# Performance work log

Measured on AMD Instinct MI355X. Metric: run time of the kernel, lower is better.

## Reference

```python
import jax, jax.numpy as jnp
import numpy as np

# 5x5 neighborhood offsets as (dx, dy), row-major as in the original delta list
DELTA = [(dx, dy) for dy in (-2, -1, 0, 1, 2) for dx in (-2, -1, 0, 1, 2)]
BN_EPS = 1e-5


def _conv(x, w, padding):
    return jax.lax.conv_general_dilated(
        x, w, window_strides=(1, 1), padding=padding,
        dimension_numbers=('NCHW', 'OIHW', 'NCHW'))


def setup_inputs() -> dict:
    key = jax.random.key(0)
    ks = jax.random.split(key, 4)
    B, C, H, W = 128, 256, 24, 24
    source_feature = jax.random.normal(ks[0], (B, C, H, W), jnp.float32)
    detection_feature = jax.random.normal(ks[1], (B, C, H, W), jnp.float32)
    w1 = jax.random.normal(ks[2], (256, 512, 3, 3), jnp.float32) * 0.02
    b1 = jnp.zeros((256,), jnp.float32)
    bn_gamma = jnp.ones((256,), jnp.float32)
    bn_beta = jnp.zeros((256,), jnp.float32)
    bn_mean = jnp.zeros((256,), jnp.float32)
    bn_var = jnp.ones((256,), jnp.float32)
    w2 = jax.random.normal(ks[3], (25, 256, 1, 1), jnp.float32) * 0.05
    b2 = jnp.zeros((25,), jnp.float32)
    return dict(source_feature=source_feature, detection_feature=detection_feature,
                w1=w1, b1=b1, bn_gamma=bn_gamma, bn_beta=bn_beta,
                bn_mean=bn_mean, bn_var=bn_var, w2=w2, b2=b2)


def reference(source_feature, detection_feature, w1, b1, bn_gamma, bn_beta,
              bn_mean, bn_var, w2, b2):
    B, C, H, W = source_feature.shape
    # kernel_pre: Conv3x3(512->256, pad 1) + BN + ReLU + Conv1x1(256->25)
    concat_f = jnp.concatenate([source_feature, detection_feature], axis=1)  # [B,512,H,W]
    x = _conv(concat_f, w1, ((1, 1), (1, 1))) + b1[None, :, None, None]
    inv = bn_gamma / jnp.sqrt(bn_var + BN_EPS)
    x = x * inv[None, :, None, None] + (bn_beta - bn_mean * inv)[None, :, None, None]
    x = jax.nn.relu(x)
    logits = _conv(x, w2, ((0, 0), (0, 0))) + b2[None, :, None, None]  # [B,25,H,W]
    # per-pixel softmax over the 25 neighborhood taps
    kmaps = jax.nn.softmax(logits, axis=1)  # [B,25,H,W]
    # propagate: softmax-weighted 5x5 neighbor gather-sum; out-of-bounds taps
    # contribute zero (matches the skipped-boundary terms in the original loop)
    padded = jnp.pad(source_feature, ((0, 0), (0, 0), (2, 2), (2, 2)))
    prop = jnp.zeros_like(source_feature)
    for order, (dx, dy) in enumerate(DELTA):
        shifted = padded[:, :, 2 + dy:2 + dy + H, 2 + dx:2 + dx + W]  # [B,C,H,W]
        prop = prop + shifted * kmaps[:, order][:, None]  # broadcast over C
    return prop
```

## Files before the change

kernel.cpp:

```cpp
#include <hip/hip_runtime.h>
#include <hip/hip_bf16.h>
#include <stdint.h>

#define BATCH 128
#define CIN   256
#define CCAT  512
#define HH    24
#define WW    24
#define HP    26
#define WP    26
#define COUT  256
#define KDIM  4608
#define NPIX  576
#define MDIM  73728
#define NORD  25

typedef __attribute__((ext_vector_type(8))) short bf16x8;
typedef __attribute__((ext_vector_type(4))) float f32x4;

__device__ __forceinline__ unsigned short f2bf(float v) {
    union { float f; unsigned u; } x; x.f = v;
    unsigned r = x.u + 0x7fffu + ((x.u >> 16) & 1u);
    return (unsigned short)(r >> 16);
}
__device__ __forceinline__ float bf_lo(unsigned w) {
    union { unsigned u; float f; } x; x.u = w << 16; return x.f;
}
__device__ __forceinline__ float bf_hi(unsigned w) {
    union { unsigned u; float f; } x; x.u = w & 0xffff0000u; return x.f;
}

__device__ __forceinline__ void async_copy16(const void* gsrc, void* ldst) {
    __builtin_amdgcn_global_load_lds(
        (const __attribute__((address_space(1))) unsigned int*)gsrc,
        (__attribute__((address_space(3))) unsigned int*)ldst, 16, 0, 0);
}

#define PTILE 192
#define LSTR  72
__global__ __launch_bounds__(256) void prep_transpose(
        const float* __restrict__ src, const float* __restrict__ det,
        unsigned short* __restrict__ apad) {
    __shared__ unsigned short lds[PTILE * LSTR];
    int pt = blockIdx.x;
    int cg = blockIdx.y;
    int b  = blockIdx.z;
    int c0 = cg * 64;
    int p0 = pt * PTILE;
    const float* inp = (c0 < CIN)
        ? (src + ((long)b * CIN + c0) * NPIX)
        : (det + ((long)b * CIN + (c0 - CIN)) * NPIX);
    int tid = threadIdx.x;

    #pragma unroll
    for (int it = 0; it < 12; it++) {
        int l  = it * 256 + tid;
        int cq = l / PTILE;
        int px = l - cq * PTILE;
        const float* pb = inp + (long)cq * 4 * NPIX + p0 + px;
        unsigned short v0 = f2bf(pb[0 * NPIX]);
        unsigned short v1 = f2bf(pb[1 * NPIX]);
        unsigned short v2 = f2bf(pb[2 * NPIX]);
        unsigned short v3 = f2bf(pb[3 * NPIX]);
        uint2 w;
        w.x = (unsigned)v0 | ((unsigned)v1 << 16);
        w.y = (unsigned)v2 | ((unsigned)v3 << 16);
        *(uint2*)&lds[px * LSTR + cq * 4] = w;
    }
    __syncthreads();

    #pragma unroll
    for (int it = 0; it < 6; it++) {
        int l   = it * 256 + tid;
        int px  = l >> 3;
        int ch8 = l & 7;
        uint4 w = *(const uint4*)&lds[px * LSTR + ch8 * 8];
        int p  = p0 + px;
        int y  = p / WW, x = p - y * WW;
        long o = (((long)b * HP + (y + 1)) * WP + (x + 1)) * CCAT + c0 + ch8 * 8;
        *(uint4*)(apad + o) = w;
    }
}

__global__ __launch_bounds__(256) void zero_halo(unsigned short* __restrict__ apad) {
    int t = blockIdx.x * 256 + threadIdx.x;
    int ch8 = t & 63;
    int r   = t >> 6;
    int hp  = r % 100;
    int b   = r / 100;
    int y, x;
    if (hp < 26)      { y = 0;       x = hp; }
    else if (hp < 52) { y = 25;      x = hp - 26; }
    else if (hp < 76) { y = hp - 51; x = 0; }
    else              { y = hp - 75; x = 25; }
    long o = (((long)b * HP + y) * WP + x) * CCAT + ch8 * 8;
    *(uint4*)(apad + o) = (uint4){0u, 0u, 0u, 0u};
}

__global__ __launch_bounds__(256) void prep_w(
        const float* __restrict__ w1, const float* __restrict__ b1,
        const float* __restrict__ gam, const float* __restrict__ bet,
        const float* __restrict__ mu, const float* __restrict__ var,
        unsigned short* __restrict__ bt,
        float* __restrict__ scale, float* __restrict__ shift) {
    int idx = blockIdx.x * 256 + threadIdx.x;
    if (idx < COUT * KDIM) {
        int n = idx / KDIM;
        int k = idx - n * KDIM;
        int s = k >> 9;
        int ci = k & 511;
        int ky = s / 3, kx = s - ky * 3;
        float v = w1[(((long)n * 512 + ci) * 3 + ky) * 3 + kx];
        bt[idx] = f2bf(v);
    }
    if (blockIdx.x == 0 && threadIdx.x < COUT) {
        int c = threadIdx.x;
        float inv = gam[c] * rsqrtf(var[c] + 1e-5f);
        scale[c] = inv;
        shift[c] = (b1[c] - mu[c]) * inv + bet[c];
    }
}

#define ABUF_SH 12288
#define BUF_SH  20480
#define STAGE_A(j, nb, soff) \
    async_copy16(apad + aSrc[j] + (soff), (void*)&lds[(nb)*BUF_SH + (j)*4096 + w*512])
#define STAGE_B(j, nb, koff) \
    async_copy16(bt + bSrc[j] + (koff), (void*)&lds[(nb)*BUF_SH + ABUF_SH + (j)*4096 + w*512])
#define BAR()  __builtin_amdgcn_s_barrier()
#define WAITV2() { asm volatile("s_waitcnt vmcnt(2)" ::: "memory"); }
#define WAITV0() { asm volatile("s_waitcnt vmcnt(0)" ::: "memory"); }
#define WAITL()  { asm volatile("s_waitcnt lgkmcnt(0)" ::: "memory"); __builtin_amdgcn_sched_barrier(0); }

__global__ __launch_bounds__(512, 2) void conv1_gemm(
        const unsigned short* __restrict__ apad,
        const unsigned short* __restrict__ bt,
        const float* __restrict__ scale, const float* __restrict__ shift,
        unsigned short* __restrict__ xout) {
    __shared__ unsigned short lds[40960];
    const int tid  = threadIdx.x;
    const int w    = tid >> 6;
    const int lane = tid & 63;
    const int wr = w >> 2, wc = w & 3;
    const int fr = lane & 15, ls = lane >> 4;

    const int Lb = blockIdx.x;
    const int logical = (Lb & 7) * 96 + (Lb >> 3);
    const int n0 = (logical & 1) * 128;
    const long m0 = (long)(logical >> 1) * 192;

    const int rowq = tid >> 3;
    const int sl   = (tid & 7) ^ (rowq & 7);
    long aSrc[3], bSrc[2];
    #pragma unroll
    for (int j = 0; j < 3; j++) {
        int r = j * 64 + rowq;
        long m = m0 + r;
        int b  = (int)(m / NPIX);
        int rr = (int)(m - (long)b * NPIX);
        int y = rr / WW, x = rr - y * WW;
        aSrc[j] = (((long)b * HP + y) * WP + x) * (long)CCAT + sl * 8;
    }
    #pragma unroll
    for (int j = 0; j < 2; j++)
        bSrc[j] = (long)(n0 + j * 64 + rowq) * KDIM + sl * 8;

    const int rb   = fr & 7;
    const int csw0 = ((ls    ) ^ rb) << 4;
    const int csw1 = ((ls + 4) ^ rb) << 4;
    const int aBase = (wr * 96 + fr) * 128;
    const int bBase = 24576 + (wc * 32 + fr) * 128;

    f32x4 acc[6][2];
    #pragma unroll
    for (int i = 0; i < 6; i++)
        #pragma unroll
        for (int j = 0; j < 2; j++) acc[i][j] = (f32x4){0.f, 0.f, 0.f, 0.f};

    STAGE_B(0, 0, 0); STAGE_B(1, 0, 0);
    STAGE_A(0, 0, 0); STAGE_A(1, 0, 0); STAGE_A(2, 0, 0);

    bf16x8 afr[3], bfr[2];
    int nb = 0;
    for (int kt = 0; kt < 71; kt++) {
        const int ktn = kt + 1;
        const int seg = ktn >> 3;
        const int ky = seg / 3, kx = seg - ky * 3;
        const long soff = (long)(ky * WP + kx) * CCAT + (ktn & 7) * 64;
        const long koff = (long)ktn * 64;
        const int pb = nb ^ 1;
        const char* L = (const char*)lds + nb * (BUF_SH * 2);

        STAGE_B(0, pb, koff); STAGE_B(1, pb, koff);
        WAITV2();
        BAR();
        #pragma unroll
        for (int n = 0; n < 2; n++)
            bfr[n] = *(const bf16x8*)(L + bBase + n * 2048 + csw0);
        #pragma unroll
        for (int m = 0; m < 3; m++)
            afr[m] = *(const bf16x8*)(L + aBase + m * 2048 + csw0);
        WAITL();
        __builtin_amdgcn_s_setprio(1);
        #pragma unroll
        for (int m = 0; m < 3; m++)
            #pragma unroll
            for (int n = 0; n < 2; n++)
                acc[m][n] = __builtin_amdgcn_mfma_f32_16x16x32_bf16(afr[m], bfr[n], acc[m][n], 0, 0, 0);
        __builtin_amdgcn_s_setprio(0);
        BAR();

        #pragma unroll
        for (int m = 0; m < 3; m++)
            afr[m] = *(const bf16x8*)(L + aBase + (3 + m) * 2048 + csw0);
        STAGE_A(0, pb, soff); STAGE_A(1, pb, soff); STAGE_A(2, pb, soff);
        WAITL();
        __builtin_amdgcn_s_setprio(1);
        #pragma unroll
        for (int m = 0; m < 3; m++)
            #pragma unroll
            for (int n = 0; n < 2; n++)
                acc[3 + m][n] = __builtin_amdgcn_mfma_f32_16x16x32_bf16(afr[m], bfr[n], acc[3 + m][n], 0, 0, 0);
        __builtin_amdgcn_s_setprio(0);
        BAR();

        #pragma unroll
        for (int n = 0; n < 2; n++)
            bfr[n] = *(const bf16x8*)(L + bBase + n * 2048 + csw1);
        #pragma unroll
        for (int m = 0; m < 3; m++)
            afr[m] = *(const bf16x8*)(L + aBase + m * 2048 + csw1);
        WAITL();
        __builtin_amdgcn_s_setprio(1);
        #pragma unroll
        for (int m = 0; m < 3; m++)
            #pragma unroll
            for (int n = 0; n < 2; n++)
                acc[m][n] = __builtin_amdgcn_mfma_f32_16x16x32_bf16(afr[m], bfr[n], acc[m][n], 0, 0, 0);
        __builtin_amdgcn_s_setprio(0);
        BAR();

        #pragma unroll
        for (int m = 0; m < 3; m++)
            afr[m] = *(const bf16x8*)(L + aBase + (3 + m) * 2048 + csw1);
        WAITL();
        __builtin_amdgcn_s_setprio(1);
        #pragma unroll
        for (int m = 0; m < 3; m++)
            #pragma unroll
            for (int n = 0; n < 2; n++)
                acc[3 + m][n] = __builtin_amdgcn_mfma_f32_16x16x32_bf16(afr[m], bfr[n], acc[3 + m][n], 0, 0, 0);
        __builtin_amdgcn_s_setprio(0);
        BAR();

        nb ^= 1;
    }

    {
        const char* L = (const char*)lds + nb * (BUF_SH * 2);
        WAITV0();
        BAR();
        #pragma unroll
        for (int n = 0; n < 2; n++)
            bfr[n] = *(const bf16x8*)(L + bBase + n * 2048 + csw0);
        #pragma unroll
        for (int m = 0; m < 3; m++)
            afr[m] = *(const bf16x8*)(L + aBase + m * 2048 + csw0);
        WAITL();
        #pragma unroll
        for (int m = 0; m < 3; m++)
            #pragma unroll
            for (int n = 0; n < 2; n++)
                acc[m][n] = __builtin_amdgcn_mfma_f32_16x16x32_bf16(afr[m], bfr[n], acc[m][n], 0, 0, 0);
        #pragma unroll
        for (int m = 0; m < 3; m++)
            afr[m] = *(const bf16x8*)(L + aBase + (3 + m) * 2048 + csw0);
        WAITL();
        #pragma unroll
        for (int m = 0; m < 3; m++)
            #pragma unroll
            for (int n = 0; n < 2; n++)
                acc[3 + m][n] = __builtin_amdgcn_mfma_f32_16x16x32_bf16(afr[m], bfr[n], acc[3 + m][n], 0, 0, 0);
        #pragma unroll
        for (int n = 0; n < 2; n++)
            bfr[n] = *(const bf16x8*)(L + bBase + n * 2048 + csw1);
        #pragma unroll
        for (int m = 0; m < 3; m++)
            afr[m] = *(const bf16x8*)(L + aBase + m * 2048 + csw1);
        WAITL();
        #pragma unroll
        for (int m = 0; m < 3; m++)
            #pragma unroll
            for (int n = 0; n < 2; n++)
                acc[m][n] = __builtin_amdgcn_mfma_f32_16x16x32_bf16(afr[m], bfr[n], acc[m][n], 0, 0, 0);
        #pragma unroll
        for (int m = 0; m < 3; m++)
            afr[m] = *(const bf16x8*)(L + aBase + (3 + m) * 2048 + csw1);
        WAITL();
        #pragma unroll
        for (int m = 0; m < 3; m++)
            #pragma unroll
            for (int n = 0; n < 2; n++)
                acc[3 + m][n] = __builtin_amdgcn_mfma_f32_16x16x32_bf16(afr[m], bfr[n], acc[3 + m][n], 0, 0, 0);
    }

    #pragma unroll
    for (int n = 0; n < 2; n++) {
        int col = n0 + wc * 32 + n * 16 + fr;
        float sc = scale[col], sh = shift[col];
        #pragma unroll
        for (int m = 0; m < 6; m++) {
            long rbase = m0 + wr * 96 + m * 16 + ls * 4;
            #pragma unroll
            for (int j = 0; j < 4; j++) {
                float v = acc[m][n][j] * sc + sh;
                v = v > 0.f ? v : 0.f;
                xout[(rbase + j) * COUT + col] = f2bf(v);
            }
        }
    }
}

__global__ __launch_bounds__(256) void conv2_softmax(
        const unsigned short* __restrict__ x, const float* __restrict__ w2,
        const float* __restrict__ b2, float* __restrict__ kmaps) {
    __shared__ float w2s[NORD * 256];
    __shared__ float b2s[NORD];
    for (int i = threadIdx.x; i < NORD * 256; i += 256) w2s[i] = w2[i];
    if (threadIdx.x < NORD) b2s[threadIdx.x] = b2[threadIdx.x];
    __syncthreads();
    long pix = (long)blockIdx.x * 256 + threadIdx.x;
    float acc[NORD];
    #pragma unroll
    for (int o = 0; o < NORD; o++) acc[o] = b2s[o];
    const unsigned short* xr = x + pix * COUT;
    for (int kc = 0; kc < 32; kc++) {
        uint4 raw = *(const uint4*)(xr + kc * 8);
        float xf[8];
        xf[0] = bf_lo(raw.x); xf[1] = bf_hi(raw.x);
        xf[2] = bf_lo(raw.y); xf[3] = bf_hi(raw.y);
        xf[4] = bf_lo(raw.z); xf[5] = bf_hi(raw.z);
        xf[6] = bf_lo(raw.w); xf[7] = bf_hi(raw.w);
        #pragma unroll
        for (int o = 0; o < NORD; o++) {
            const float* wrow = &w2s[o * 256 + kc * 8];
            float4 wa = *(const float4*)(wrow);
            float4 wb = *(const float4*)(wrow + 4);
            acc[o] += xf[0] * wa.x + xf[1] * wa.y + xf[2] * wa.z + xf[3] * wa.w
                    + xf[4] * wb.x + xf[5] * wb.y + xf[6] * wb.z + xf[7] * wb.w;
        }
    }
    float mx = acc[0];
    #pragma unroll
    for (int o = 1; o < NORD; o++) mx = fmaxf(mx, acc[o]);
    float s = 0.f;
    #pragma unroll
    for (int o = 0; o < NORD; o++) { acc[o] = expf(acc[o] - mx); s += acc[o]; }
    float inv = 1.f / s;
    float* kout = kmaps + pix * NORD;
    #pragma unroll
    for (int o = 0; o < NORD; o++) kout[o] = acc[o] * inv;
}

__global__ __launch_bounds__(576) void propagate(
        const float* __restrict__ src, const float* __restrict__ kmaps,
        float* __restrict__ out) {
    __shared__ float sm[28 * 28];
    int b  = blockIdx.y;
    int cg = blockIdx.x;
    int tid = threadIdx.x;
    int y = tid / 24, x = tid - y * 24;
    float km[NORD];
    const float* kp = kmaps + ((long)b * NPIX + tid) * NORD;
    #pragma unroll
    for (int o = 0; o < NORD; o++) km[o] = kp[o];
    for (int c = 0; c < 16; c++) {
        int cc = cg * 16 + c;
        const float* sp = src + ((long)b * CIN + cc) * NPIX;
        __syncthreads();
        for (int t = tid; t < 28 * 28; t += 576) {
            int yy = t / 28, xx = t - yy * 28;
            float v = 0.f;
            if (yy >= 2 && yy < 26 && xx >= 2 && xx < 26)
                v = sp[(yy - 2) * 24 + (xx - 2)];
            sm[t] = v;
        }
        __syncthreads();
        float a = 0.f;
        #pragma unroll
        for (int o = 0; o < NORD; o++) {
            int dy = o / 5 - 2, dx = o % 5 - 2;
            a += km[o] * sm[(y + 2 + dy) * 28 + (x + 2 + dx)];
        }
        out[((long)b * CIN + cc) * NPIX + tid] = a;
    }
}

extern "C" void kernel_launch(void* const* d_in, const int* in_sizes, int n_in,
                              void* d_out, int out_size, void* d_ws, size_t ws_size,
                              hipStream_t stream) {
    const float* src = (const float*)d_in[0];
    const float* det = (const float*)d_in[1];
    const float* w1  = (const float*)d_in[2];
    const float* b1  = (const float*)d_in[3];
    const float* gam = (const float*)d_in[4];
    const float* bet = (const float*)d_in[5];
    const float* mu  = (const float*)d_in[6];
    const float* var = (const float*)d_in[7];
    const float* w2  = (const float*)d_in[8];
    const float* b2  = (const float*)d_in[9];
    float* out = (float*)d_out;

    char* ws = (char*)d_ws;
    size_t off = 0;
    unsigned short* apad = (unsigned short*)(ws + off); off += (size_t)BATCH * HP * WP * CCAT * 2;
    unsigned short* bt   = (unsigned short*)(ws + off); off += (size_t)COUT * KDIM * 2;
    unsigned short* xbuf = (unsigned short*)(ws + off); off += (size_t)MDIM * COUT * 2;
    float* kmaps = (float*)(ws + off); off += (size_t)MDIM * NORD * 4;
    float* scale = (float*)(ws + off); off += 1024;
    float* shift = (float*)(ws + off); off += 1024;

    zero_halo<<<3200, 256, 0, stream>>>(apad);
    prep_transpose<<<dim3(3, 8, BATCH), 256, 0, stream>>>(src, det, apad);
    prep_w<<<4608, 256, 0, stream>>>(w1, b1, gam, bet, mu, var, bt, scale, shift);
    conv1_gemm<<<768, 512, 0, stream>>>(apad, bt, scale, shift, xbuf);
    conv2_softmax<<<288, 256, 0, stream>>>(xbuf, w2, b2, kmaps);
    propagate<<<dim3(16, BATCH), 576, 0, stream>>>(src, kmaps, out);
}
```

Measured before the change: 358.7 us.

## Fold halo zeroing into prep, transpose kmaps layout, batch propagate channels

Halo zeroing moves into the prep_transpose kernel, which removes one launch. kmaps is now stored order-major so that per-pixel reads in propagate coalesce. propagate stages 8 channels per shared-memory round with 64 channels per block, cutting barriers and raising memory-level parallelism. In exchange the grid shrinks to 512 blocks and shared memory use grows, which may reduce occupancy.

```diff
diff --git a/kernel.cpp b/kernel.cpp
--- a/kernel.cpp
+++ b/kernel.cpp
@@ -52,6 +52,24 @@
         : (det + ((long)b * CIN + (c0 - CIN)) * NPIX);
     int tid = threadIdx.x;
 
+    if (pt == 0) {
+        #pragma unroll
+        for (int it = 0; it < 4; it++) {
+            int t = it * 256 + tid;
+            if (t < 800) {
+                int ch8 = t & 7;
+                int hp  = t >> 3;
+                int y, x;
+                if (hp < 26)      { y = 0;       x = hp; }
+                else if (hp < 52) { y = 25;      x = hp - 26; }
+                else if (hp < 76) { y = hp - 51; x = 0; }
+                else              { y = hp - 75; x = 25; }
+                long o = (((long)b * HP + y) * WP + x) * CCAT + c0 + ch8 * 8;
+                *(uint4*)(apad + o) = (uint4){0u, 0u, 0u, 0u};
+            }
+        }
+    }
+
     #pragma unroll
     for (int it = 0; it < 12; it++) {
         int l  = it * 256 + tid;
@@ -80,21 +98,6 @@
         long o = (((long)b * HP + (y + 1)) * WP + (x + 1)) * CCAT + c0 + ch8 * 8;
         *(uint4*)(apad + o) = w;
     }
-}
-
-__global__ __launch_bounds__(256) void zero_halo(unsigned short* __restrict__ apad) {
-    int t = blockIdx.x * 256 + threadIdx.x;
-    int ch8 = t & 63;
-    int r   = t >> 6;
-    int hp  = r % 100;
-    int b   = r / 100;
-    int y, x;
-    if (hp < 26)      { y = 0;       x = hp; }
-    else if (hp < 52) { y = 25;      x = hp - 26; }
-    else if (hp < 76) { y = hp - 51; x = 0; }
-    else              { y = hp - 75; x = 25; }
-    long o = (((long)b * HP + y) * WP + x) * CCAT + ch8 * 8;
-    *(uint4*)(apad + o) = (uint4){0u, 0u, 0u, 0u};
 }
 
 __global__ __launch_bounds__(256) void prep_w(
@@ -357,42 +360,44 @@
     #pragma unroll
     for (int o = 0; o < NORD; o++) { acc[o] = expf(acc[o] - mx); s += acc[o]; }
     float inv = 1.f / s;
-    float* kout = kmaps + pix * NORD;
-    #pragma unroll
-    for (int o = 0; o < NORD; o++) kout[o] = acc[o] * inv;
+    #pragma unroll
+    for (int o = 0; o < NORD; o++) kmaps[(long)o * MDIM + pix] = acc[o] * inv;
 }
 
 __global__ __launch_bounds__(576) void propagate(
         const float* __restrict__ src, const float* __restrict__ kmaps,
         float* __restrict__ out) {
-    __shared__ float sm[28 * 28];
+    __shared__ float sm[8][28 * 28];
     int b  = blockIdx.y;
     int cg = blockIdx.x;
     int tid = threadIdx.x;
     int y = tid / 24, x = tid - y * 24;
+    long pixg = (long)b * NPIX + tid;
     float km[NORD];
-    const float* kp = kmaps + ((long)b * NPIX + tid) * NORD;
-    #pragma unroll
-    for (int o = 0; o < NORD; o++) km[o] = kp[o];
-    for (int c = 0; c < 16; c++) {
-        int cc = cg * 16 + c;
-        const float* sp = src + ((long)b * CIN + cc) * NPIX;
+    #pragma unroll
+    for (int o = 0; o < NORD; o++) km[o] = kmaps[(long)o * MDIM + pixg];
+    for (int r = 0; r < 8; r++) {
+        int cbase = cg * 64 + r * 8;
         __syncthreads();
-        for (int t = tid; t < 28 * 28; t += 576) {
-            int yy = t / 28, xx = t - yy * 28;
+        for (int t = tid; t < 8 * 784; t += 576) {
+            int cp = t / 784, u = t - cp * 784;
+            int yy = u / 28, xx = u - yy * 28;
             float v = 0.f;
             if (yy >= 2 && yy < 26 && xx >= 2 && xx < 26)
-                v = sp[(yy - 2) * 24 + (xx - 2)];
-            sm[t] = v;
+                v = src[((long)b * CIN + cbase + cp) * NPIX + (yy - 2) * 24 + (xx - 2)];
+            sm[cp][u] = v;
         }
         __syncthreads();
-        float a = 0.f;
-        #pragma unroll
-        for (int o = 0; o < NORD; o++) {
-            int dy = o / 5 - 2, dx = o % 5 - 2;
-            a += km[o] * sm[(y + 2 + dy) * 28 + (x + 2 + dx)];
+        #pragma unroll
+        for (int cp = 0; cp < 8; cp++) {
+            float a = 0.f;
+            #pragma unroll
+            for (int o = 0; o < NORD; o++) {
+                int dy = o / 5 - 2, dx = o % 5 - 2;
+                a += km[o] * sm[cp][(y + 2 + dy) * 28 + (x + 2 + dx)];
+            }
+            out[((long)b * CIN + cbase + cp) * NPIX + tid] = a;
         }
-        out[((long)b * CIN + cc) * NPIX + tid] = a;
     }
 }
 
@@ -420,10 +425,9 @@
     float* scale = (float*)(ws + off); off += 1024;
     float* shift = (float*)(ws + off); off += 1024;
 
-    zero_halo<<<3200, 256, 0, stream>>>(apad);
     prep_transpose<<<dim3(3, 8, BATCH), 256, 0, stream>>>(src, det, apad);
     prep_w<<<4608, 256, 0, stream>>>(w1, b1, gam, bet, mu, var, bt, scale, shift);
     conv1_gemm<<<768, 512, 0, stream>>>(apad, bt, scale, shift, xbuf);
     conv2_softmax<<<288, 256, 0, stream>>>(xbuf, w2, b2, kmaps);
-    propagate<<<dim3(16, BATCH), 576, 0, stream>>>(src, kmaps, out);
-}
+    propagate<<<dim3(4, BATCH), 576, 0, stream>>>(src, kmaps, out);
+}
```

After: 396.0 us. +10.4%, slower.
